# Kernel optimization log

Hardware: AMD Instinct MI355X
Metric: run time of the kernel (lower is better)

Reference implementation:

```python
import jax, jax.numpy as jnp
import numpy as np

D, F, E, K = 1024, 2048, 8, 2
EPS = 1.1920929e-07  # torch.finfo(float32).eps, RMSNorm default eps=None


def setup_inputs() -> dict:
    key = jax.random.key(0)
    ks = jax.random.split(key, 6)
    x = jax.random.normal(ks[0], (2, 2048, D), jnp.float32)
    Wg = jax.random.normal(ks[1], (D, E), jnp.float32)          # Gate.weights ~ randn
    norm_w = jnp.ones((E, D), jnp.float32)                       # per-expert RMSNorm weight
    W1 = jax.random.normal(ks[2], (E, D, F), jnp.float32) * 0.02
    b1 = jnp.zeros((E, F), jnp.float32)
    W2 = jax.random.normal(ks[3], (E, D, F), jnp.float32) * 0.02
    b2 = jnp.zeros((E, F), jnp.float32)
    W3 = jax.random.normal(ks[4], (E, F, D), jnp.float32) * 0.02
    b3 = jnp.zeros((E, D), jnp.float32)
    return {"x": x, "Wg": Wg, "norm_w": norm_w, "W1": W1, "b1": b1,
            "W2": W2, "b2": b2, "W3": W3, "b3": b3, "k": K}


def reference(x, Wg, norm_w, W1, b1, W2, b2, W3, b3, k):
    orig_shape = x.shape
    xt = x.reshape(-1, x.shape[-1])                    # [T, d]
    num_experts = Wg.shape[-1]

    # --- Gate: top-k then softmax over selected logits ---
    scores = xt @ Wg                                   # [T, E]
    top_v, top_i = jax.lax.top_k(scores, k)            # [T, k]
    gates = jax.nn.softmax(top_v, axis=-1)             # [T, k]
    # combine weight per (token, expert); zero for unrouted experts
    comb = jnp.einsum('tk,tke->te', gates,
                      jax.nn.one_hot(top_i, num_experts, dtype=gates.dtype))  # [T, E]

    # --- Per-expert SwiGLU FFN with RMSNorm (norm weight folded into W1/W2) ---
    inv = jax.lax.rsqrt(jnp.mean(xt * xt, axis=-1, keepdims=True) + EPS)
    xh = xt * inv                                      # [T, d] (un-weighted RMSNorm)
    W1p = norm_w[:, :, None] * W1                      # [E, d, f]
    W2p = norm_w[:, :, None] * W2
    a = jnp.einsum('td,edf->etf', xh, W1p) + b1[:, None, :]   # [E, T, f]
    g = jnp.einsum('td,edf->etf', xh, W2p) + b2[:, None, :]
    h = jax.nn.silu(a) * g                             # [E, T, f]
    o = jnp.einsum('etf,efd->etd', h, W3) + b3[:, None, :]    # [E, T, d]

    # --- Weighted combine (comb==0 for unrouted -> identical to masked loop) ---
    y = jnp.einsum('etd,te->td', o, comb)              # [T, d]
    return y.reshape(orig_shape)
```

## Files before the change

kernel.cpp:

```cpp
#include <hip/hip_runtime.h>
#include <hip/hip_bf16.h>

typedef unsigned short u16;
typedef __attribute__((ext_vector_type(8))) short bf16x8;
typedef __attribute__((ext_vector_type(4))) float f32x4;

#define D_DIM 1024
#define F_DIM 2048
#define E_NUM 8
#define EPS_RMS 1.1920929e-07f
#define NCHUNK 16

__device__ __forceinline__ u16 f2bf(float f) {
  union { float f; unsigned u; } v; v.f = f;
  unsigned r = v.u + 0x7FFFu + ((v.u >> 16) & 1u);
  return (u16)(r >> 16);
}

__device__ __forceinline__ void async16(const void* g, void* l) {
  __builtin_amdgcn_global_load_lds((const __attribute__((address_space(1))) void*)g,
                                   (__attribute__((address_space(3))) void*)l, 16, 0, 0);
}

__global__ __launch_bounds__(256) void prep_kernel(
    const float* __restrict__ W1, const float* __restrict__ W2,
    const float* __restrict__ W3, const float* __restrict__ scale,
    const float* __restrict__ x, const float* __restrict__ Wg,
    u16* __restrict__ Wc, u16* __restrict__ W3t, u16* __restrict__ xh,
    int* __restrict__ topi, float* __restrict__ gatev)
{
  __shared__ float tile[64][65];
  __shared__ float red[4][9];
  __shared__ float invs;
  const int lin = blockIdx.x;
  const int tid = threadIdx.x;

  if (lin < 8192) {
    const int z = lin >> 9;
    const int rem = lin & 511;
    const int cb = (rem & 31) * 64;
    const int rb = (rem >> 5) * 64;
    const int e = z & 7;
    const float* W = (z < 8) ? W1 : W2;
    const int gofs = (z < 8) ? 0 : 16;
    const int tx = tid & 15, ty = tid >> 4;
    const float* Wp = W + (size_t)e * D_DIM * F_DIM;
#pragma unroll
    for (int rep = 0; rep < 4; ++rep) {
      const int i = ty + rep * 16;
      float4 v = *reinterpret_cast<const float4*>(Wp + (size_t)(rb + i) * F_DIM + cb + tx * 4);
      tile[i][tx*4+0] = v.x; tile[i][tx*4+1] = v.y; tile[i][tx*4+2] = v.z; tile[i][tx*4+3] = v.w;
    }
    __syncthreads();
    float sc[4];
#pragma unroll
    for (int q = 0; q < 4; ++q) sc[q] = scale[(size_t)e * D_DIM + rb + tx*4 + q];
    u16* op = Wc + (size_t)e * (2*F_DIM) * D_DIM;
#pragma unroll
    for (int rep = 0; rep < 4; ++rep) {
      const int j = ty + rep * 16;
      const int c = cb + j;
      const int rphys = ((c >> 4) << 5) + (c & 15) + gofs;
      ushort4 o;
      o.x = f2bf(tile[tx*4+0][j] * sc[0]);
      o.y = f2bf(tile[tx*4+1][j] * sc[1]);
      o.z = f2bf(tile[tx*4+2][j] * sc[2]);
      o.w = f2bf(tile[tx*4+3][j] * sc[3]);
      *reinterpret_cast<ushort4*>(op + (size_t)rphys * D_DIM + rb + tx*4) = o;
    }
  } else if (lin < 12288) {
    const int l2 = lin - 8192;
    const int e = l2 >> 9;
    const int rem = l2 & 511;
    const int cb = (rem & 15) * 64;
    const int rb = (rem >> 4) * 64;
    const int tx = tid & 15, ty = tid >> 4;
    const float* Wp = W3 + (size_t)e * F_DIM * D_DIM;
#pragma unroll
    for (int rep = 0; rep < 4; ++rep) {
      const int i = ty + rep * 16;
      float4 v = *reinterpret_cast<const float4*>(Wp + (size_t)(rb + i) * D_DIM + cb + tx * 4);
      tile[i][tx*4+0] = v.x; tile[i][tx*4+1] = v.y; tile[i][tx*4+2] = v.z; tile[i][tx*4+3] = v.w;
    }
    __syncthreads();
    u16* op = W3t + (size_t)e * F_DIM * D_DIM;
#pragma unroll
    for (int rep = 0; rep < 4; ++rep) {
      const int j = ty + rep * 16;
      ushort4 o;
      o.x = f2bf(tile[tx*4+0][j]);
      o.y = f2bf(tile[tx*4+1][j]);
      o.z = f2bf(tile[tx*4+2][j]);
      o.w = f2bf(tile[tx*4+3][j]);
      *reinterpret_cast<ushort4*>(op + (size_t)(cb + j) * F_DIM + rb + tx*4) = o;
    }
  } else {
    const int t = lin - 12288;
    const float4 xv = reinterpret_cast<const float4*>(x + (size_t)t * D_DIM)[tid];
    float ss = xv.x*xv.x + xv.y*xv.y + xv.z*xv.z + xv.w*xv.w;
    float s[8];
#pragma unroll
    for (int e = 0; e < 8; ++e) s[e] = 0.f;
    const float xa[4] = {xv.x, xv.y, xv.z, xv.w};
#pragma unroll
    for (int j = 0; j < 4; ++j) {
      const float4* wr = reinterpret_cast<const float4*>(Wg + (size_t)(tid*4 + j) * 8);
      float4 w0 = wr[0], w1 = wr[1];
      s[0] += xa[j]*w0.x; s[1] += xa[j]*w0.y; s[2] += xa[j]*w0.z; s[3] += xa[j]*w0.w;
      s[4] += xa[j]*w1.x; s[5] += xa[j]*w1.y; s[6] += xa[j]*w1.z; s[7] += xa[j]*w1.w;
    }
#pragma unroll
    for (int off = 32; off > 0; off >>= 1) {
      ss += __shfl_down(ss, off);
#pragma unroll
      for (int e = 0; e < 8; ++e) s[e] += __shfl_down(s[e], off);
    }
    const int wv = tid >> 6, lane = tid & 63;
    if (lane == 0) { red[wv][8] = ss;
#pragma unroll
      for (int e = 0; e < 8; ++e) red[wv][e] = s[e]; }
    __syncthreads();
    if (tid == 0) {
      float sum2 = red[0][8] + red[1][8] + red[2][8] + red[3][8];
      invs = rsqrtf(sum2 * (1.0f / D_DIM) + EPS_RMS);
      float sc[8];
#pragma unroll
      for (int e = 0; e < 8; ++e) sc[e] = red[0][e] + red[1][e] + red[2][e] + red[3][e];
      int i0 = 0; float v0 = sc[0];
#pragma unroll
      for (int e = 1; e < 8; ++e) if (sc[e] > v0) { v0 = sc[e]; i0 = e; }
      int i1 = -1; float v1 = -3.0e38f;
#pragma unroll
      for (int e = 0; e < 8; ++e) if (e != i0 && sc[e] > v1) { v1 = sc[e]; i1 = e; }
      float p1 = 1.0f / (1.0f + expf(v0 - v1));
      float p0 = 1.0f - p1;
      topi[2*t] = i0; topi[2*t+1] = i1;
      gatev[2*t] = p0; gatev[2*t+1] = p1;
    }
    __syncthreads();
    const float inv = invs;
    ushort4 o;
    o.x = f2bf(xv.x*inv); o.y = f2bf(xv.y*inv); o.z = f2bf(xv.z*inv); o.w = f2bf(xv.w*inv);
    reinterpret_cast<ushort4*>(xh + (size_t)t * D_DIM)[tid] = o;
  }
}

__global__ __launch_bounds__(256) void count_kernel(
    const int* __restrict__ topi, int* __restrict__ percnt, int nent)
{
  const int blk = blockIdx.x;
  const int tid = threadIdx.x;
  const int per = (nent + NCHUNK*256 - 1) / (NCHUNK*256);
  const int cbase = blk * 256 * per;
  int c[8];
#pragma unroll
  for (int q = 0; q < 8; ++q) c[q] = 0;
  for (int i = 0; i < per; ++i) {
    const int idx = cbase + tid * per + i;
    if (idx < nent) {
      const int e = topi[idx];
#pragma unroll
      for (int q = 0; q < 8; ++q) c[q] += (e == q) ? 1 : 0;
    }
  }
#pragma unroll
  for (int off = 32; off > 0; off >>= 1)
#pragma unroll
    for (int q = 0; q < 8; ++q) c[q] += __shfl_down(c[q], off);
  __shared__ int red[4][8];
  const int wv = tid >> 6, lane = tid & 63;
  if (lane == 0)
#pragma unroll
    for (int q = 0; q < 8; ++q) red[wv][q] = c[q];
  __syncthreads();
  if (tid < 8) percnt[blk * 8 + tid] = red[0][tid] + red[1][tid] + red[2][tid] + red[3][tid];
}

__global__ __launch_bounds__(256) void scatter_kernel(
    const int* __restrict__ topi, const int* __restrict__ percnt,
    int* __restrict__ rowtok, int* __restrict__ slots, int* __restrict__ offs, int nent)
{
  __shared__ int cur[8];
  const int blk = blockIdx.x, tid = threadIdx.x;
  if (tid == 0) {
    int tot[8];
#pragma unroll
    for (int e = 0; e < 8; ++e) {
      tot[e] = 0;
      for (int c = 0; c < NCHUNK; ++c) tot[e] += percnt[c*8 + e];
    }
    int acc = 0, start[8];
#pragma unroll
    for (int e = 0; e < 8; ++e) {
      start[e] = acc;
      if (blk == 0) offs[e] = acc;
      acc += (tot[e] + 255) & ~255;
    }
    if (blk == 0) offs[8] = acc;
    for (int c = 0; c < blk; ++c)
#pragma unroll
      for (int e = 0; e < 8; ++e) start[e] += percnt[c*8 + e];
#pragma unroll
    for (int e = 0; e < 8; ++e) cur[e] = start[e];
  }
  __syncthreads();
  const int per = (nent + NCHUNK*256 - 1) / (NCHUNK*256);
  const int cbase = blk * 256 * per;
  for (int i = 0; i < per; ++i) {
    const int idx = cbase + tid * per + i;
    if (idx < nent) {
      const int e = topi[idx];
      const int pos = atomicAdd(&cur[e], 1);
      rowtok[pos] = idx >> 1;
      slots[idx] = pos;
    }
  }
}

__global__ __launch_bounds__(512, 4) void ffn1_kernel(
    const u16* __restrict__ xh, const u16* __restrict__ Wc,
    const float* __restrict__ b1, const float* __restrict__ b2,
    const int* __restrict__ rowtok, const int* __restrict__ offs,
    u16* __restrict__ h)
{
  __shared__ __align__(16) u16 smem[36864];

  const int row0 = blockIdx.y * 256;
  if (row0 >= offs[8]) return;
  int e = 0;
#pragma unroll
  for (int i = 1; i < 8; ++i) e += (row0 >= offs[i]) ? 1 : 0;

  const int bx = blockIdx.x;
  const int n0p = bx * 128;
  const int tid = threadIdx.x;
  const int lane = tid & 63;
  const int l15 = lane & 15;
  const int wv = tid >> 6;
  const int wm = wv >> 1;
  const int wn = wv & 1;

  int arow[2];
  const u16* gAp[2];
#pragma unroll
  for (int j = 0; j < 2; ++j) {
    const int i = tid + 512*j;
    const int p = i >> 3;
    const int v = (i & 7) ^ (p & 7);
    arow[j] = 2*p + (v >> 2);
    int tk = rowtok[row0 + arow[j]];
    if (tk < 0) tk = 0;
    gAp[j] = xh + (size_t)tk * D_DIM + (v & 3) * 8;
  }
  const u16* gBp;
  {
    const int i = tid;
    const int p = i >> 3;
    const int v = (i & 7) ^ (p & 7);
    const int brow = 2*p + (v >> 2);
    gBp = Wc + ((size_t)e * (2*F_DIM) + n0p + brow) * D_DIM + (v & 3) * 8;
  }

  const f32x4 zero = {0.f, 0.f, 0.f, 0.f};
  f32x4 acc[4][4];
#pragma unroll
  for (int i = 0; i < 4; ++i)
#pragma unroll
    for (int j = 0; j < 4; ++j) acc[i][j] = zero;

  const int rlane = (((l15 & 1) << 2) + (lane >> 4)) ^ (l15 >> 1);
  const int aoff = (l15 >> 1) * 64 + rlane * 8;
  const int boff = (l15 >> 1) * 64 + rlane * 8;

#define STAGE1(b, k0)                                                       \
  {                                                                         \
    const int base_ = (b) * 12288;                                          \
    async16(gAp[0] + (k0), &smem[base_ + tid*8]);                           \
    async16(gAp[1] + (k0), &smem[base_ + (tid + 512)*8]);                   \
    async16(gBp   + (k0), &smem[base_ + 8192 + tid*8]);                     \
  }

  STAGE1(0, 0);
  STAGE1(1, 32);

  const int NSTEP = D_DIM / 32;
  for (int t = 0; t < NSTEP; ++t) {
    const int bsel = t % 3;
    if (t + 1 < NSTEP) {
      asm volatile("s_waitcnt vmcnt(3)" ::: "memory");
    } else {
      asm volatile("s_waitcnt vmcnt(0)" ::: "memory");
    }
    __builtin_amdgcn_s_barrier();
    if (t + 2 < NSTEP) {
      const int bn = (t + 2) % 3;
      const int kn = (t + 2) * 32;
      STAGE1(bn, kn);
    }
    const int aB = bsel * 12288, bB = aB + 8192;
    bf16x8 af[4], bv[4];
#pragma unroll
    for (int mi = 0; mi < 4; ++mi)
      af[mi] = *(const bf16x8*)(&smem[aB + (wm*32 + mi*8)*64 + aoff]);
#pragma unroll
    for (int ni = 0; ni < 4; ++ni)
      bv[ni] = *(const bf16x8*)(&smem[bB + (wn*32 + ni*8)*64 + boff]);
#pragma unroll
    for (int mi = 0; mi < 4; ++mi)
#pragma unroll
      for (int ni = 0; ni < 4; ++ni)
        acc[mi][ni] = __builtin_amdgcn_mfma_f32_16x16x32_bf16(af[mi], bv[ni], acc[mi][ni], 0, 0, 0);
  }
#undef STAGE1

#pragma unroll
  for (int mi = 0; mi < 4; ++mi) {
    const int rbase = row0 + wm*64 + mi*16 + (lane >> 4)*4;
#pragma unroll
    for (int q = 0; q < 2; ++q) {
      const int rc = bx*64 + wn*32 + q*16 + l15;
      const float bb1 = b1[e*F_DIM + rc], bb2 = b2[e*F_DIM + rc];
#pragma unroll
      for (int r = 0; r < 4; ++r) {
        float a = acc[mi][2*q][r] + bb1;
        float g = acc[mi][2*q+1][r] + bb2;
        h[(size_t)(rbase + r) * F_DIM + rc] = f2bf(a / (1.f + __expf(-a)) * g);
      }
    }
  }
}

__global__ __launch_bounds__(256, 2) void ffn2_kernel(
    const u16* __restrict__ h, const u16* __restrict__ W3t,
    const float* __restrict__ b3, const int* __restrict__ offs,
    float* __restrict__ opart)
{
  __shared__ __align__(16) u16 smem[32768];

  const int lin = blockIdx.y * gridDim.x + blockIdx.x;
  const int qc  = (gridDim.x * gridDim.y) >> 3;
  const int L   = (lin & 7) * qc + (lin >> 3);
  const int bx  = L % gridDim.x;
  const int by  = L / gridDim.x;

  const int row0 = by * 128;
  if (row0 >= offs[8]) return;
  int e = 0;
#pragma unroll
  for (int i = 1; i < 8; ++i) e += (row0 >= offs[i]) ? 1 : 0;

  const int n0 = bx * 128;
  const int tid = threadIdx.x;
  const int lane = tid & 63;
  const int wv = tid >> 6;
  const int wm = wv >> 1;
  const int wn = wv & 1;

  const int srow = tid >> 3;
  const int sseg = (tid & 7) ^ (srow & 7);
  const u16* gA[4]; const u16* gB[4];
#pragma unroll
  for (int j = 0; j < 4; ++j) {
    gA[j] = h   + (size_t)(row0 + srow + 32*j) * F_DIM + sseg * 8;
    gB[j] = W3t + ((size_t)e * D_DIM + n0 + srow + 32*j) * F_DIM + sseg * 8;
  }

  const f32x4 zero = {0.f, 0.f, 0.f, 0.f};
  f32x4 acc[4][4];
#pragma unroll
  for (int i = 0; i < 4; ++i)
#pragma unroll
    for (int j = 0; j < 4; ++j) acc[i][j] = zero;

  const int rswz = (lane & 7) << 3;
  const int kpart = (lane >> 4) * 8;
  const int arowbase = (wm*64 + (lane & 15)) * 64;
  const int browbase = (wn*64 + (lane & 15)) * 64;

#define STAGE2(b, k0)                                                       \
  {                                                                         \
    const int aB_ = (b)*8192, bB_ = 16384 + (b)*8192;                       \
    _Pragma("unroll")                                                       \
    for (int j = 0; j < 4; ++j) {                                           \
      async16(gA[j] + (k0), &smem[aB_ + (tid + 256*j)*8]);                  \
      async16(gB[j] + (k0), &smem[bB_ + (tid + 256*j)*8]);                  \
    }                                                                       \
  }

  STAGE2(0, 0);
  __syncthreads();

  int cur = 0;
  for (int t = 0; t < F_DIM/64; ++t) {
    if (t + 1 < F_DIM/64) STAGE2(cur ^ 1, (t+1)*64);
    const int aB = cur*8192, bB = 16384 + cur*8192;
#pragma unroll
    for (int kk = 0; kk < 2; ++kk) {
      const int ko = kk*32 + kpart;
      bf16x8 af[4], bv[4];
#pragma unroll
      for (int mi = 0; mi < 4; ++mi)
        af[mi] = *(const bf16x8*)(&smem[aB + ((arowbase + mi*1024 + ko) ^ rswz)]);
#pragma unroll
      for (int ni = 0; ni < 4; ++ni)
        bv[ni] = *(const bf16x8*)(&smem[bB + ((browbase + ni*1024 + ko) ^ rswz)]);
#pragma unroll
      for (int mi = 0; mi < 4; ++mi)
#pragma unroll
        for (int ni = 0; ni < 4; ++ni)
          acc[mi][ni] = __builtin_amdgcn_mfma_f32_16x16x32_bf16(af[mi], bv[ni], acc[mi][ni], 0, 0, 0);
    }
    __syncthreads();
    cur ^= 1;
  }
#undef STAGE2

#pragma unroll
  for (int mi = 0; mi < 4; ++mi) {
    const int rbase = row0 + wm*64 + mi*16 + (lane >> 4)*4;
#pragma unroll
    for (int ni = 0; ni < 4; ++ni) {
      const int gc = n0 + wn*64 + ni*16 + (lane & 15);
      const float bb = b3[e*D_DIM + gc];
#pragma unroll
      for (int r = 0; r < 4; ++r)
        opart[(size_t)(rbase + r) * D_DIM + gc] = acc[mi][ni][r] + bb;
    }
  }
}

__global__ __launch_bounds__(256) void combine_kernel(
    const float* __restrict__ opart, const int* __restrict__ slots,
    const float* __restrict__ gatev, float* __restrict__ y)
{
  const int t = blockIdx.x;
  const int s0 = slots[2*t], s1 = slots[2*t+1];
  const float w0 = gatev[2*t], w1 = gatev[2*t+1];
  const float4 a = reinterpret_cast<const float4*>(opart + (size_t)s0 * D_DIM)[threadIdx.x];
  const float4 b = reinterpret_cast<const float4*>(opart + (size_t)s1 * D_DIM)[threadIdx.x];
  float4 o;
  o.x = w0*a.x + w1*b.x; o.y = w0*a.y + w1*b.y;
  o.z = w0*a.z + w1*b.z; o.w = w0*a.w + w1*b.w;
  reinterpret_cast<float4*>(y + (size_t)t * D_DIM)[threadIdx.x] = o;
}

extern "C" void kernel_launch(void* const* d_in, const int* in_sizes, int n_in,
                              void* d_out, int out_size, void* d_ws, size_t ws_size,
                              hipStream_t stream)
{
  const float* x  = (const float*)d_in[0];
  const float* Wg = (const float*)d_in[1];
  const float* nw = (const float*)d_in[2];
  const float* W1 = (const float*)d_in[3];
  const float* b1 = (const float*)d_in[4];
  const float* W2 = (const float*)d_in[5];
  const float* b2 = (const float*)d_in[6];
  const float* W3 = (const float*)d_in[7];
  const float* b3 = (const float*)d_in[8];
  float* y = (float*)d_out;

  const int T = in_sizes[0] / D_DIM;
  const int NENT = T * 2;
  const int RCAP = ((NENT + E_NUM * 255) + 255) & ~255;
  const int MT1 = RCAP / 256;
  const int MT2 = RCAP / 128;

  char* ws = (char*)d_ws;
  size_t off_ = 0;
  auto take = [&](size_t bytes) { char* p = ws + off_; off_ = (off_ + bytes + 255) & ~(size_t)255; return p; };
  u16* Wc     = (u16*)take((size_t)E_NUM * 2 * F_DIM * D_DIM * 2);
  u16* W3t    = (u16*)take((size_t)E_NUM * D_DIM * F_DIM * 2);
  u16* xh     = (u16*)take((size_t)T * D_DIM * 2);
  u16* hbuf   = (u16*)take((size_t)RCAP * F_DIM * 2);
  int* rowtok = (int*)take((size_t)RCAP * 4);
  int* slots  = (int*)take((size_t)NENT * 4);
  int* topi   = (int*)take((size_t)NENT * 4);
  float* gatev= (float*)take((size_t)NENT * 4);
  int* percnt = (int*)take(NCHUNK * 8 * 4);
  int* offs   = (int*)take(64);
  float* opart = (float*)Wc;
  (void)ws_size; (void)n_in; (void)out_size;

  hipMemsetAsync(rowtok, 0xFF, (size_t)RCAP * 4, stream);

  prep_kernel<<<12288 + T, 256, 0, stream>>>(W1, W2, W3, nw, x, Wg, Wc, W3t, xh, topi, gatev);
  count_kernel<<<NCHUNK, 256, 0, stream>>>(topi, percnt, NENT);
  scatter_kernel<<<NCHUNK, 256, 0, stream>>>(topi, percnt, rowtok, slots, offs, NENT);

  ffn1_kernel<<<dim3((2*F_DIM)/128, MT1), 512, 0, stream>>>(xh, Wc, b1, b2, rowtok, offs, hbuf);
  ffn2_kernel<<<dim3(D_DIM/128, MT2), 256, 0, stream>>>(hbuf, W3t, b3, offs, opart);
  combine_kernel<<<T, 256, 0, stream>>>(opart, slots, gatev, y);
}
```

Measured before the change: 233.6 us.

## Triple-buffer ffn2 K=32 stages and batch weight-transpose loads in prep

ffn2 moves from a double-buffered K=64 tile to a triple-buffered K=32 pipeline. It uses a new swizzled LDS layout, waits on vmcnt with a single barrier per step, and shrinks LDS so four blocks can fit per CU instead of two. The prep kernel now has each block transpose four 64x64 tiles, issuing all global loads into registers up front, which cuts the block count and raises memory-level parallelism. The risks are more iterations and barriers in ffn2, higher register pressure under the tighter launch bound, and extra syncs in prep.

```diff
diff --git a/kernel.cpp b/kernel.cpp
--- a/kernel.cpp
+++ b/kernel.cpp
@@ -34,68 +34,92 @@
   __shared__ float invs;
   const int lin = blockIdx.x;
   const int tid = threadIdx.x;
-
-  if (lin < 8192) {
-    const int z = lin >> 9;
-    const int rem = lin & 511;
-    const int cb = (rem & 31) * 64;
-    const int rb = (rem >> 5) * 64;
+  const int tx = tid & 15, ty = tid >> 4;
+
+  if (lin < 2048) {
+    const int z = lin >> 7;
+    const int rem = lin & 127;
+    const int cb = (rem & 7) * 256;
+    const int rb = (rem >> 3) * 64;
     const int e = z & 7;
     const float* W = (z < 8) ? W1 : W2;
     const int gofs = (z < 8) ? 0 : 16;
-    const int tx = tid & 15, ty = tid >> 4;
     const float* Wp = W + (size_t)e * D_DIM * F_DIM;
-#pragma unroll
-    for (int rep = 0; rep < 4; ++rep) {
-      const int i = ty + rep * 16;
-      float4 v = *reinterpret_cast<const float4*>(Wp + (size_t)(rb + i) * F_DIM + cb + tx * 4);
-      tile[i][tx*4+0] = v.x; tile[i][tx*4+1] = v.y; tile[i][tx*4+2] = v.z; tile[i][tx*4+3] = v.w;
-    }
-    __syncthreads();
+    float4 v[4][4];
+#pragma unroll
+    for (int r = 0; r < 4; ++r) {
+      const float* rowp = Wp + (size_t)(rb + ty + r*16) * F_DIM + cb;
+#pragma unroll
+      for (int s = 0; s < 4; ++s)
+        v[r][s] = *reinterpret_cast<const float4*>(rowp + s*64 + tx*4);
+    }
     float sc[4];
 #pragma unroll
     for (int q = 0; q < 4; ++q) sc[q] = scale[(size_t)e * D_DIM + rb + tx*4 + q];
     u16* op = Wc + (size_t)e * (2*F_DIM) * D_DIM;
 #pragma unroll
-    for (int rep = 0; rep < 4; ++rep) {
-      const int j = ty + rep * 16;
-      const int c = cb + j;
-      const int rphys = ((c >> 4) << 5) + (c & 15) + gofs;
-      ushort4 o;
-      o.x = f2bf(tile[tx*4+0][j] * sc[0]);
-      o.y = f2bf(tile[tx*4+1][j] * sc[1]);
-      o.z = f2bf(tile[tx*4+2][j] * sc[2]);
-      o.w = f2bf(tile[tx*4+3][j] * sc[3]);
-      *reinterpret_cast<ushort4*>(op + (size_t)rphys * D_DIM + rb + tx*4) = o;
-    }
-  } else if (lin < 12288) {
-    const int l2 = lin - 8192;
-    const int e = l2 >> 9;
-    const int rem = l2 & 511;
-    const int cb = (rem & 15) * 64;
-    const int rb = (rem >> 4) * 64;
-    const int tx = tid & 15, ty = tid >> 4;
+    for (int s = 0; s < 4; ++s) {
+#pragma unroll
+      for (int r = 0; r < 4; ++r) {
+        const int i = ty + r*16;
+        tile[i][tx*4+0] = v[r][s].x; tile[i][tx*4+1] = v[r][s].y;
+        tile[i][tx*4+2] = v[r][s].z; tile[i][tx*4+3] = v[r][s].w;
+      }
+      __syncthreads();
+#pragma unroll
+      for (int rep = 0; rep < 4; ++rep) {
+        const int j = ty + rep*16;
+        const int c = cb + s*64 + j;
+        const int rphys = ((c >> 4) << 5) + (c & 15) + gofs;
+        ushort4 o;
+        o.x = f2bf(tile[tx*4+0][j] * sc[0]);
+        o.y = f2bf(tile[tx*4+1][j] * sc[1]);
+        o.z = f2bf(tile[tx*4+2][j] * sc[2]);
+        o.w = f2bf(tile[tx*4+3][j] * sc[3]);
+        *reinterpret_cast<ushort4*>(op + (size_t)rphys * D_DIM + rb + tx*4) = o;
+      }
+      __syncthreads();
+    }
+  } else if (lin < 3072) {
+    const int l2 = lin - 2048;
+    const int e = l2 >> 7;
+    const int rem = l2 & 127;
+    const int db = (rem & 3) * 256;
+    const int rbF = (rem >> 2) * 64;
     const float* Wp = W3 + (size_t)e * F_DIM * D_DIM;
-#pragma unroll
-    for (int rep = 0; rep < 4; ++rep) {
-      const int i = ty + rep * 16;
-      float4 v = *reinterpret_cast<const float4*>(Wp + (size_t)(rb + i) * D_DIM + cb + tx * 4);
-      tile[i][tx*4+0] = v.x; tile[i][tx*4+1] = v.y; tile[i][tx*4+2] = v.z; tile[i][tx*4+3] = v.w;
-    }
-    __syncthreads();
+    float4 v[4][4];
+#pragma unroll
+    for (int r = 0; r < 4; ++r) {
+      const float* rowp = Wp + (size_t)(rbF + ty + r*16) * D_DIM + db;
+#pragma unroll
+      for (int s = 0; s < 4; ++s)
+        v[r][s] = *reinterpret_cast<const float4*>(rowp + s*64 + tx*4);
+    }
     u16* op = W3t + (size_t)e * F_DIM * D_DIM;
 #pragma unroll
-    for (int rep = 0; rep < 4; ++rep) {
-      const int j = ty + rep * 16;
-      ushort4 o;
-      o.x = f2bf(tile[tx*4+0][j]);
-      o.y = f2bf(tile[tx*4+1][j]);
-      o.z = f2bf(tile[tx*4+2][j]);
-      o.w = f2bf(tile[tx*4+3][j]);
-      *reinterpret_cast<ushort4*>(op + (size_t)(cb + j) * F_DIM + rb + tx*4) = o;
+    for (int s = 0; s < 4; ++s) {
+#pragma unroll
+      for (int r = 0; r < 4; ++r) {
+        const int i = ty + r*16;
+        tile[i][tx*4+0] = v[r][s].x; tile[i][tx*4+1] = v[r][s].y;
+        tile[i][tx*4+2] = v[r][s].z; tile[i][tx*4+3] = v[r][s].w;
+      }
+      __syncthreads();
+#pragma unroll
+      for (int rep = 0; rep < 4; ++rep) {
+        const int j = ty + rep*16;
+        const int d = db + s*64 + j;
+        ushort4 o;
+        o.x = f2bf(tile[tx*4+0][j]);
+        o.y = f2bf(tile[tx*4+1][j]);
+        o.z = f2bf(tile[tx*4+2][j]);
+        o.w = f2bf(tile[tx*4+3][j]);
+        *reinterpret_cast<ushort4*>(op + (size_t)d * F_DIM + rbF + tx*4) = o;
+      }
+      __syncthreads();
     }
   } else {
-    const int t = lin - 12288;
+    const int t = lin - 3072;
     const float4 xv = reinterpret_cast<const float4*>(x + (size_t)t * D_DIM)[tid];
     float ss = xv.x*xv.x + xv.y*xv.y + xv.z*xv.z + xv.w*xv.w;
     float s[8];
@@ -330,12 +354,12 @@
   }
 }
 
-__global__ __launch_bounds__(256, 2) void ffn2_kernel(
+__global__ __launch_bounds__(256, 4) void ffn2_kernel(
     const u16* __restrict__ h, const u16* __restrict__ W3t,
     const float* __restrict__ b3, const int* __restrict__ offs,
     float* __restrict__ opart)
 {
-  __shared__ __align__(16) u16 smem[32768];
+  __shared__ __align__(16) u16 smem[24576];
 
   const int lin = blockIdx.y * gridDim.x + blockIdx.x;
   const int qc  = (gridDim.x * gridDim.y) >> 3;
@@ -352,17 +376,21 @@
   const int n0 = bx * 128;
   const int tid = threadIdx.x;
   const int lane = tid & 63;
+  const int l15 = lane & 15;
   const int wv = tid >> 6;
   const int wm = wv >> 1;
   const int wn = wv & 1;
 
-  const int srow = tid >> 3;
-  const int sseg = (tid & 7) ^ (srow & 7);
-  const u16* gA[4]; const u16* gB[4];
-#pragma unroll
-  for (int j = 0; j < 4; ++j) {
-    gA[j] = h   + (size_t)(row0 + srow + 32*j) * F_DIM + sseg * 8;
-    gB[j] = W3t + ((size_t)e * D_DIM + n0 + srow + 32*j) * F_DIM + sseg * 8;
+  const u16* gAp[2]; const u16* gBp[2];
+#pragma unroll
+  for (int j = 0; j < 2; ++j) {
+    const int i = tid + 256*j;
+    const int p = i >> 3;
+    const int v = (i & 7) ^ (p & 7);
+    const int row = 2*p + (v >> 2);
+    const int seg = v & 3;
+    gAp[j] = h   + (size_t)(row0 + row) * F_DIM + seg * 8;
+    gBp[j] = W3t + ((size_t)e * D_DIM + n0 + row) * F_DIM + seg * 8;
   }
 
   const f32x4 zero = {0.f, 0.f, 0.f, 0.f};
@@ -372,46 +400,46 @@
 #pragma unroll
     for (int j = 0; j < 4; ++j) acc[i][j] = zero;
 
-  const int rswz = (lane & 7) << 3;
-  const int kpart = (lane >> 4) * 8;
-  const int arowbase = (wm*64 + (lane & 15)) * 64;
-  const int browbase = (wn*64 + (lane & 15)) * 64;
+  const int rlane = (((l15 & 1) << 2) + (lane >> 4)) ^ (l15 >> 1);
+  const int roff = (l15 >> 1) * 64 + rlane * 8;
 
 #define STAGE2(b, k0)                                                       \
   {                                                                         \
-    const int aB_ = (b)*8192, bB_ = 16384 + (b)*8192;                       \
-    _Pragma("unroll")                                                       \
-    for (int j = 0; j < 4; ++j) {                                           \
-      async16(gA[j] + (k0), &smem[aB_ + (tid + 256*j)*8]);                  \
-      async16(gB[j] + (k0), &smem[bB_ + (tid + 256*j)*8]);                  \
-    }                                                                       \
+    const int base_ = (b) * 8192;                                           \
+    async16(gAp[0] + (k0), &smem[base_ + tid*8]);                           \
+    async16(gAp[1] + (k0), &smem[base_ + (tid + 256)*8]);                   \
+    async16(gBp[0] + (k0), &smem[base_ + 4096 + tid*8]);                    \
+    async16(gBp[1] + (k0), &smem[base_ + 4096 + (tid + 256)*8]);            \
   }
 
   STAGE2(0, 0);
-  __syncthreads();
-
-  int cur = 0;
-  for (int t = 0; t < F_DIM/64; ++t) {
-    if (t + 1 < F_DIM/64) STAGE2(cur ^ 1, (t+1)*64);
-    const int aB = cur*8192, bB = 16384 + cur*8192;
-#pragma unroll
-    for (int kk = 0; kk < 2; ++kk) {
-      const int ko = kk*32 + kpart;
-      bf16x8 af[4], bv[4];
-#pragma unroll
-      for (int mi = 0; mi < 4; ++mi)
-        af[mi] = *(const bf16x8*)(&smem[aB + ((arowbase + mi*1024 + ko) ^ rswz)]);
+  STAGE2(1, 32);
+
+  const int NSTEP = F_DIM / 32;
+  for (int t = 0; t < NSTEP; ++t) {
+    const int bsel = t % 3;
+    if (t + 1 < NSTEP) {
+      asm volatile("s_waitcnt vmcnt(4)" ::: "memory");
+    } else {
+      asm volatile("s_waitcnt vmcnt(0)" ::: "memory");
+    }
+    __builtin_amdgcn_s_barrier();
+    if (t + 2 < NSTEP) {
+      STAGE2((t + 2) % 3, (t + 2) * 32);
+    }
+    const int aB = bsel * 8192, bB = aB + 4096;
+    bf16x8 af[4], bv[4];
+#pragma unroll
+    for (int mi = 0; mi < 4; ++mi)
+      af[mi] = *(const bf16x8*)(&smem[aB + (wm*32 + mi*8)*64 + roff]);
+#pragma unroll
+    for (int ni = 0; ni < 4; ++ni)
+      bv[ni] = *(const bf16x8*)(&smem[bB + (wn*32 + ni*8)*64 + roff]);
+#pragma unroll
+    for (int mi = 0; mi < 4; ++mi)
 #pragma unroll
       for (int ni = 0; ni < 4; ++ni)
-        bv[ni] = *(const bf16x8*)(&smem[bB + ((browbase + ni*1024 + ko) ^ rswz)]);
-#pragma unroll
-      for (int mi = 0; mi < 4; ++mi)
-#pragma unroll
-        for (int ni = 0; ni < 4; ++ni)
-          acc[mi][ni] = __builtin_amdgcn_mfma_f32_16x16x32_bf16(af[mi], bv[ni], acc[mi][ni], 0, 0, 0);
-    }
-    __syncthreads();
-    cur ^= 1;
+        acc[mi][ni] = __builtin_amdgcn_mfma_f32_16x16x32_bf16(af[mi], bv[ni], acc[mi][ni], 0, 0, 0);
   }
 #undef STAGE2
 
@@ -420,7 +448,7 @@
     const int rbase = row0 + wm*64 + mi*16 + (lane >> 4)*4;
 #pragma unroll
     for (int ni = 0; ni < 4; ++ni) {
-      const int gc = n0 + wn*64 + ni*16 + (lane & 15);
+      const int gc = n0 + wn*64 + ni*16 + l15;
       const float bb = b3[e*D_DIM + gc];
 #pragma unroll
       for (int r = 0; r < 4; ++r)
@@ -481,9 +509,9 @@
   float* opart = (float*)Wc;
   (void)ws_size; (void)n_in; (void)out_size;
 
-  hipMemsetAsync(rowtok, 0xFF, (size_t)RCAP * 4, stream);
-
-  prep_kernel<<<12288 + T, 256, 0, stream>>>(W1, W2, W3, nw, x, Wg, Wc, W3t, xh, topi, gatev);
+  (void)hipMemsetAsync(rowtok, 0xFF, (size_t)RCAP * 4, stream);
+
+  prep_kernel<<<3072 + T, 256, 0, stream>>>(W1, W2, W3, nw, x, Wg, Wc, W3t, xh, topi, gatev);
   count_kernel<<<NCHUNK, 256, 0, stream>>>(topi, percnt, NENT);
   scatter_kernel<<<NCHUNK, 256, 0, stream>>>(topi, percnt, rowtok, slots, offs, NENT);
 
```

Result: slower. 246.0 us (+5.3%).

## Move W3 transpose-convert from prep kernel into extra ffn1 blocks

Applied to the files above, without the earlier changes.

The W3 fp32-to-bf16 transpose work is taken out of prep_kernel and placed in 64 extra rows of ffn1 blocks. Each of these blocks handles two 64x64 tiles using its 512 threads. The goal is to overlap this memory-bound conversion with the ffn1 GEMM blocks and to shorten the critical path through prep, count and scatter. The risk is that the extra blocks compete with the GEMM blocks for CUs and bandwidth, or get scheduled after the GEMM blocks in grid order.

```diff
diff --git a/kernel.cpp b/kernel.cpp
--- a/kernel.cpp
+++ b/kernel.cpp
@@ -24,9 +24,9 @@
 
 __global__ __launch_bounds__(256) void prep_kernel(
     const float* __restrict__ W1, const float* __restrict__ W2,
-    const float* __restrict__ W3, const float* __restrict__ scale,
+    const float* __restrict__ scale,
     const float* __restrict__ x, const float* __restrict__ Wg,
-    u16* __restrict__ Wc, u16* __restrict__ W3t, u16* __restrict__ xh,
+    u16* __restrict__ Wc, u16* __restrict__ xh,
     int* __restrict__ topi, float* __restrict__ gatev)
 {
   __shared__ float tile[64][65];
@@ -68,34 +68,8 @@
       o.w = f2bf(tile[tx*4+3][j] * sc[3]);
       *reinterpret_cast<ushort4*>(op + (size_t)rphys * D_DIM + rb + tx*4) = o;
     }
-  } else if (lin < 12288) {
-    const int l2 = lin - 8192;
-    const int e = l2 >> 9;
-    const int rem = l2 & 511;
-    const int cb = (rem & 15) * 64;
-    const int rb = (rem >> 4) * 64;
-    const int tx = tid & 15, ty = tid >> 4;
-    const float* Wp = W3 + (size_t)e * F_DIM * D_DIM;
-#pragma unroll
-    for (int rep = 0; rep < 4; ++rep) {
-      const int i = ty + rep * 16;
-      float4 v = *reinterpret_cast<const float4*>(Wp + (size_t)(rb + i) * D_DIM + cb + tx * 4);
-      tile[i][tx*4+0] = v.x; tile[i][tx*4+1] = v.y; tile[i][tx*4+2] = v.z; tile[i][tx*4+3] = v.w;
-    }
-    __syncthreads();
-    u16* op = W3t + (size_t)e * F_DIM * D_DIM;
-#pragma unroll
-    for (int rep = 0; rep < 4; ++rep) {
-      const int j = ty + rep * 16;
-      ushort4 o;
-      o.x = f2bf(tile[tx*4+0][j]);
-      o.y = f2bf(tile[tx*4+1][j]);
-      o.z = f2bf(tile[tx*4+2][j]);
-      o.w = f2bf(tile[tx*4+3][j]);
-      *reinterpret_cast<ushort4*>(op + (size_t)(cb + j) * F_DIM + rb + tx*4) = o;
-    }
   } else {
-    const int t = lin - 12288;
+    const int t = lin - 8192;
     const float4 xv = reinterpret_cast<const float4*>(x + (size_t)t * D_DIM)[tid];
     float ss = xv.x*xv.x + xv.y*xv.y + xv.z*xv.z + xv.w*xv.w;
     float s[8];
@@ -219,11 +193,48 @@
 
 __global__ __launch_bounds__(512, 4) void ffn1_kernel(
     const u16* __restrict__ xh, const u16* __restrict__ Wc,
+    const float* __restrict__ W3, u16* __restrict__ W3t,
     const float* __restrict__ b1, const float* __restrict__ b2,
     const int* __restrict__ rowtok, const int* __restrict__ offs,
-    u16* __restrict__ h)
+    u16* __restrict__ h, int MT1)
 {
   __shared__ __align__(16) u16 smem[36864];
+
+  const int tid = threadIdx.x;
+
+  if ((int)blockIdx.y >= MT1) {
+    float* ftile = reinterpret_cast<float*>(smem);
+    const int half = tid >> 8;
+    const int t8 = tid & 255;
+    const int tx = t8 & 15, ty = t8 >> 4;
+    const int tileIdx = ((int)blockIdx.y - MT1) * 64 + (int)blockIdx.x * 2 + half;
+    const int e = tileIdx >> 9;
+    const int rem = tileIdx & 511;
+    const int cb = (rem & 15) * 64;
+    const int rb = (rem >> 4) * 64;
+    float* tl = ftile + half * 64 * 65;
+    const float* Wp = W3 + (size_t)e * F_DIM * D_DIM;
+#pragma unroll
+    for (int rep = 0; rep < 4; ++rep) {
+      const int i = ty + rep * 16;
+      float4 v = *reinterpret_cast<const float4*>(Wp + (size_t)(rb + i) * D_DIM + cb + tx * 4);
+      tl[i*65 + tx*4+0] = v.x; tl[i*65 + tx*4+1] = v.y;
+      tl[i*65 + tx*4+2] = v.z; tl[i*65 + tx*4+3] = v.w;
+    }
+    __syncthreads();
+    u16* op = W3t + (size_t)e * D_DIM * F_DIM;
+#pragma unroll
+    for (int rep = 0; rep < 4; ++rep) {
+      const int j = ty + rep * 16;
+      ushort4 o;
+      o.x = f2bf(tl[(tx*4+0)*65 + j]);
+      o.y = f2bf(tl[(tx*4+1)*65 + j]);
+      o.z = f2bf(tl[(tx*4+2)*65 + j]);
+      o.w = f2bf(tl[(tx*4+3)*65 + j]);
+      *reinterpret_cast<ushort4*>(op + (size_t)(cb + j) * F_DIM + rb + tx*4) = o;
+    }
+    return;
+  }
 
   const int row0 = blockIdx.y * 256;
   if (row0 >= offs[8]) return;
@@ -233,7 +244,6 @@
 
   const int bx = blockIdx.x;
   const int n0p = bx * 128;
-  const int tid = threadIdx.x;
   const int lane = tid & 63;
   const int l15 = lane & 15;
   const int wv = tid >> 6;
@@ -481,13 +491,14 @@
   float* opart = (float*)Wc;
   (void)ws_size; (void)n_in; (void)out_size;
 
-  hipMemsetAsync(rowtok, 0xFF, (size_t)RCAP * 4, stream);
-
-  prep_kernel<<<12288 + T, 256, 0, stream>>>(W1, W2, W3, nw, x, Wg, Wc, W3t, xh, topi, gatev);
+  (void)hipMemsetAsync(rowtok, 0xFF, (size_t)RCAP * 4, stream);
+
+  prep_kernel<<<8192 + T, 256, 0, stream>>>(W1, W2, nw, x, Wg, Wc, xh, topi, gatev);
   count_kernel<<<NCHUNK, 256, 0, stream>>>(topi, percnt, NENT);
   scatter_kernel<<<NCHUNK, 256, 0, stream>>>(topi, percnt, rowtok, slots, offs, NENT);
 
-  ffn1_kernel<<<dim3((2*F_DIM)/128, MT1), 512, 0, stream>>>(xh, Wc, b1, b2, rowtok, offs, hbuf);
+  ffn1_kernel<<<dim3((2*F_DIM)/128, MT1 + 64), 512, 0, stream>>>(
+      xh, Wc, W3, W3t, b1, b2, rowtok, offs, hbuf, MT1);
   ffn2_kernel<<<dim3(D_DIM/128, MT2), 256, 0, stream>>>(hbuf, W3t, b3, offs, opart);
   combine_kernel<<<T, 256, 0, stream>>>(opart, slots, gatev, y);
 }
```

After: 224.9 us (median of 2 runs). 3.7% less time.
